# Optimization experiments

Hardware: AMD Instinct MI355X
Metric: run time of the kernel (lower is better)

The kernel has to match this reference:

```python
import jax, jax.numpy as jnp
import numpy as np
import math

JOINT_NAMES = ['pelvis', 'hip_R', 'hip_L', 'knee_R', 'knee_L', 'ankle_R', 'ankle_L', 'trunk', 'shoulder_R', 'shoulder_L', 'elbow_R', 'elbow_L']
KINEMATIC_CHAINS = {'pelvis': ['hip_R', 'hip_L', 'trunk'], 'hip_R': ['pelvis', 'knee_R'], 'hip_L': ['pelvis', 'knee_L'], 'knee_R': ['hip_R', 'ankle_R'], 'knee_L': ['hip_L', 'ankle_L'], 'ankle_R': ['knee_R'], 'ankle_L': ['knee_L'], 'trunk': ['pelvis', 'shoulder_R', 'shoulder_L'], 'shoulder_R': ['trunk', 'elbow_R'], 'shoulder_L': ['trunk', 'elbow_L'], 'elbow_R': ['shoulder_R'], 'elbow_L': ['shoulder_L']}

D_MODEL = 128
N_HEADS = 4
HEAD_DIM = D_MODEL // N_HEADS
B = 16384
N = 12

def build_adjacency_matrix():
    n = len(JOINT_NAMES)
    adj = np.zeros((n, n), dtype=np.float32)
    idx = {name: i for i, name in enumerate(JOINT_NAMES)}
    for joint, neighbors in KINEMATIC_CHAINS.items():
        i = idx[joint]
        for nb in neighbors:
            j = idx[nb]
            adj[i, j] = 1.0
            adj[j, i] = 1.0
    adj = adj + np.eye(n, dtype=np.float32)
    return jnp.asarray(adj)

def setup_inputs() -> dict:
    key = jax.random.key(0)
    ks = jax.random.split(key, 12)
    s = 1.0 / math.sqrt(D_MODEL)  # torch Linear default init scale
    inp = {
        'x': jax.random.normal(ks[0], (B, N, D_MODEL), dtype=jnp.float32),
        'visibility': jax.random.uniform(ks[1], (B, N), dtype=jnp.float32),
        'Wq': jax.random.uniform(ks[2], (D_MODEL, D_MODEL), jnp.float32, -s, s),
        'bq': jax.random.uniform(ks[3], (D_MODEL,), jnp.float32, -s, s),
        'Wk': jax.random.uniform(ks[4], (D_MODEL, D_MODEL), jnp.float32, -s, s),
        'bk': jax.random.uniform(ks[5], (D_MODEL,), jnp.float32, -s, s),
        'Wv': jax.random.uniform(ks[6], (D_MODEL, D_MODEL), jnp.float32, -s, s),
        'bv': jax.random.uniform(ks[7], (D_MODEL,), jnp.float32, -s, s),
        'Wo': jax.random.uniform(ks[8], (D_MODEL, D_MODEL), jnp.float32, -s, s),
        'bo': jax.random.uniform(ks[9], (D_MODEL,), jnp.float32, -s, s),
        'bias_scale': jnp.asarray(1.0, dtype=jnp.float32),
        'adjacency': build_adjacency_matrix(),
    }
    return inp

def reference(x, visibility, Wq, bq, Wk, bk, Wv, bv, Wo, bo, bias_scale, adjacency):
    Bsz, Nj, D = x.shape
    # projections; weights stored as (out,in) like torch Linear -> x @ W.T + b
    def proj(W, b):
        return (jnp.einsum('bnd,ed->bne', x, W) + b).reshape(Bsz, Nj, N_HEADS, HEAD_DIM).transpose(0, 2, 1, 3)
    q = proj(Wq, bq)  # (B, H, N, hd)
    k = proj(Wk, bk)
    v = proj(Wv, bv)
    scores = jnp.einsum('bhnd,bhmd->bhnm', q, k) / math.sqrt(HEAD_DIM)
    scores = scores + adjacency[None, None, :, :] * bias_scale
    # visibility mask: subtract 10 where key joint is not visible
    scores = scores - 10.0 * (1.0 - visibility[:, None, None, :])
    attn = jax.nn.softmax(scores, axis=-1)
    out = jnp.einsum('bhnm,bhmd->bhnd', attn, v)
    out = out.transpose(0, 2, 1, 3).reshape(Bsz, Nj, D)
    out = jnp.einsum('bnd,ed->bne', out, Wo) + bo
    return out
```

## Files before the change

### kernel.cpp

```cpp
#include <hip/hip_runtime.h>


typedef unsigned short u16;
typedef short bf16x8 __attribute__((ext_vector_type(8)));
typedef short bf16x4 __attribute__((ext_vector_type(4)));
typedef float f32x4 __attribute__((ext_vector_type(4)));

#define MFMA(a, b, c) __builtin_amdgcn_mfma_f32_16x16x32_bf16((a), (b), (c), 0, 0, 0)

#define BPW   4
#define ROWS  (BPW * 12)
#define XPAD  136
#define VPAD  20
#define PPAD  20

struct SMem {
    u16   qs[ROWS * XPAD];
    u16   ks[ROWS * XPAD];
    u16   vT[BPW * 128 * VPAD];
    u16   P[4 * 16 * PPAD];
    float bias_s[16 * 16];
    float vis_s[BPW * 16];
    float bvec[4 * 128];
    float rls[4 * 16];
};

__device__ __forceinline__ u16 f2b(float f) {
    unsigned u = __builtin_bit_cast(unsigned, f);
    return (u16)((u + 0x7fffu + ((u >> 16) & 1u)) >> 16);
}

__device__ __forceinline__ void st4(u16* p, float a, float b, float c, float d) {
    ushort4 v; v.x = f2b(a); v.y = f2b(b); v.z = f2b(c); v.w = f2b(d);
    *(ushort4*)p = v;
}

__device__ __forceinline__ bf16x8 pack8(float4 a, float4 b) {
    bf16x8 r;
    r[0] = (short)f2b(a.x); r[1] = (short)f2b(a.y);
    r[2] = (short)f2b(a.z); r[3] = (short)f2b(a.w);
    r[4] = (short)f2b(b.x); r[5] = (short)f2b(b.y);
    r[6] = (short)f2b(b.z); r[7] = (short)f2b(b.w);
    return r;
}

__global__ void prep_w(const float* __restrict__ Wq, const float* __restrict__ Wk,
                       const float* __restrict__ Wv, const float* __restrict__ Wo,
                       u16* __restrict__ wbf) {
    int i = blockIdx.x * 256 + threadIdx.x;
    wbf[i]         = f2b(Wq[i]);
    wbf[16384 + i] = f2b(Wk[i]);
    wbf[32768 + i] = f2b(Wv[i]);
    wbf[49152 + i] = f2b(Wo[i]);
}

__global__ __launch_bounds__(256, 3) void cja_main(
    const float* __restrict__ x, const float* __restrict__ vis,
    const float* __restrict__ bq, const float* __restrict__ bk,
    const float* __restrict__ bv, const float* __restrict__ bo,
    const float* __restrict__ bias_scale, const float* __restrict__ adj,
    const u16* __restrict__ wbf, float* __restrict__ out)
{
    extern __shared__ char smraw[];
    SMem& sm = *(SMem*)smraw;

    const int tid  = threadIdx.x;
    const int wave = tid >> 6;
    const int lane = tid & 63;
    const int lq   = lane >> 4;
    const int lm   = lane & 15;
    const int b0   = blockIdx.x * BPW;

    for (int i = tid; i < BPW * 128; i += 256) {
        unsigned* d = (unsigned*)(sm.vT + i * VPAD + 12);
        d[0] = 0u; d[1] = 0u; d[2] = 0u; d[3] = 0u;
    }
    {
        const float L2E = 1.4426950408889634f;
        float scale = bias_scale[0] * L2E;
        int n = tid >> 4, m = tid & 15;
        float bval;
        if (m >= 12)     bval = -1e30f;
        else if (n < 12) bval = adj[n * 12 + m] * scale;
        else             bval = 0.0f;
        sm.bias_s[tid] = bval;
        if (tid < BPW * 16) {
            int bb = tid >> 4, mm = tid & 15;
            sm.vis_s[tid] = (mm < 12) ? 10.0f * L2E * (1.0f - vis[(size_t)(b0 + bb) * 12 + mm])
                                      : 0.0f;
        }
        if (tid < 128) {
            sm.bvec[tid]       = bq[tid];
            sm.bvec[128 + tid] = bk[tid];
            sm.bvec[256 + tid] = bv[tid];
            sm.bvec[384 + tid] = bo[tid];
        }
    }
    __syncthreads();

    {
        const u16* Wq_b = wbf;
        const u16* Wk_b = wbf + 16384;
        const u16* Wv_b = wbf + 32768;
        const float* xw = x + (size_t)b0 * 1536;
        f32x4 accq[2][3], acck[2][3], accv[3][2];
        #pragma unroll
        for (int i = 0; i < 2; i++)
            #pragma unroll
            for (int j = 0; j < 3; j++) { accq[i][j] = (f32x4){0,0,0,0}; acck[i][j] = (f32x4){0,0,0,0}; }
        #pragma unroll
        for (int i = 0; i < 3; i++)
            #pragma unroll
            for (int j = 0; j < 2; j++) accv[i][j] = (f32x4){0,0,0,0};

        const int mrow0 = wave * 32 + lm;
        const int mrow1 = mrow0 + 16;
        #pragma unroll
        for (int ks2 = 0; ks2 < 4; ks2++) {
            const int koff = ks2 * 32 + lq * 8;
            bf16x8 xf[3];
            #pragma unroll
            for (int nt = 0; nt < 3; nt++) {
                const float* xp = xw + (nt * 16 + lm) * 128 + koff;
                float4 u0 = *(const float4*)xp;
                float4 u1 = *(const float4*)(xp + 4);
                xf[nt] = pack8(u0, u1);
            }
            bf16x8 wq0 = *(const bf16x8*)(Wq_b + mrow0 * 128 + koff);
            bf16x8 wq1 = *(const bf16x8*)(Wq_b + mrow1 * 128 + koff);
            bf16x8 wk0 = *(const bf16x8*)(Wk_b + mrow0 * 128 + koff);
            bf16x8 wk1 = *(const bf16x8*)(Wk_b + mrow1 * 128 + koff);
            bf16x8 wv0 = *(const bf16x8*)(Wv_b + mrow0 * 128 + koff);
            bf16x8 wv1 = *(const bf16x8*)(Wv_b + mrow1 * 128 + koff);
            #pragma unroll
            for (int nt = 0; nt < 3; nt++) {
                accq[0][nt] = MFMA(wq0, xf[nt], accq[0][nt]);
                accq[1][nt] = MFMA(wq1, xf[nt], accq[1][nt]);
                acck[0][nt] = MFMA(wk0, xf[nt], acck[0][nt]);
                acck[1][nt] = MFMA(wk1, xf[nt], acck[1][nt]);
                accv[nt][0] = MFMA(xf[nt], wv0, accv[nt][0]);
                accv[nt][1] = MFMA(xf[nt], wv1, accv[nt][1]);
            }
        }
        #pragma unroll
        for (int mi = 0; mi < 2; mi++) {
            const int e0 = (wave * 2 + mi) * 16 + lq * 4;
            float bq0 = sm.bvec[e0], bq1 = sm.bvec[e0+1], bq2 = sm.bvec[e0+2], bq3 = sm.bvec[e0+3];
            float bk0 = sm.bvec[128+e0], bk1 = sm.bvec[128+e0+1], bk2 = sm.bvec[128+e0+2], bk3 = sm.bvec[128+e0+3];
            #pragma unroll
            for (int nt = 0; nt < 3; nt++) {
                const int n = nt * 16 + lm;
                st4(sm.qs + n * XPAD + e0, accq[mi][nt][0]+bq0, accq[mi][nt][1]+bq1,
                                           accq[mi][nt][2]+bq2, accq[mi][nt][3]+bq3);
                st4(sm.ks + n * XPAD + e0, acck[mi][nt][0]+bk0, acck[mi][nt][1]+bk1,
                                           acck[mi][nt][2]+bk2, acck[mi][nt][3]+bk3);
            }
        }
        #pragma unroll
        for (int nt2 = 0; nt2 < 2; nt2++) {
            const int e = (wave * 2 + nt2) * 16 + lm;
            const float bvv = sm.bvec[256 + e];
            #pragma unroll
            for (int mt = 0; mt < 3; mt++) {
                #pragma unroll
                for (int r = 0; r < 4; r++) {
                    int n = mt * 16 + lq * 4 + r;
                    int bb = n / 12, j = n - bb * 12;
                    sm.vT[bb * (128 * VPAD) + e * VPAD + j] = f2b(accv[mt][nt2][r] + bvv);
                }
            }
        }
    }
    __syncthreads();

    {
        const int bl   = wave;
        const int nql  = (lm < 12) ? lm : 11;
        const u16* qrowp = sm.qs + (bl * 12 + nql) * XPAD;
        const u16* krowp = sm.ks + (bl * 12 + nql) * XPAD;
        const float vism = sm.vis_s[bl * 16 + lm];
        float bias_b[4];
        #pragma unroll
        for (int r = 0; r < 4; r++) bias_b[r] = sm.bias_s[(lq * 4 + r) * 16 + lm];
        u16*   Pw  = sm.P + wave * (16 * PPAD);
        float* rlw = sm.rls + wave * 16;
        const u16* vTb = sm.vT + bl * (128 * VPAD);
        const float SC2 = 0.2550348606381560f;
        const bf16x8 z8 = {0,0,0,0,0,0,0,0};
        #pragma unroll
        for (int h = 0; h < 4; h++) {
            bf16x8 qa = *(const bf16x8*)(qrowp + h * 32 + lq * 8);
            bf16x8 kb = *(const bf16x8*)(krowp + h * 32 + lq * 8);
            f32x4 sc = MFMA(qa, kb, ((f32x4){0,0,0,0}));
            #pragma unroll
            for (int r = 0; r < 4; r++) {
                float s2 = sc[r] * SC2 + bias_b[r] - vism;
                float e  = __builtin_amdgcn_exp2f(s2);
                float l  = e;
                l += __shfl_xor(l, 1, 16);
                l += __shfl_xor(l, 2, 16);
                l += __shfl_xor(l, 4, 16);
                l += __shfl_xor(l, 8, 16);
                Pw[(lq * 4 + r) * PPAD + lm] = f2b(e);
                if (lm == 0) rlw[lq * 4 + r] = __builtin_amdgcn_rcpf(l);
            }
            float rln = rlw[lm];
            bf16x8 pb = z8;
            if (lq < 2) {
                const bf16x4* pp = (const bf16x4*)(Pw + lm * PPAD + lq * 8);
                pb = __builtin_shufflevector(pp[0], pp[1], 0, 1, 2, 3, 4, 5, 6, 7);
            }
            #pragma unroll
            for (int mt = 0; mt < 2; mt++) {
                bf16x8 va = z8;
                if (lq < 2) {
                    const bf16x4* vp = (const bf16x4*)(vTb + (h * 32 + mt * 16 + lm) * VPAD + lq * 8);
                    va = __builtin_shufflevector(vp[0], vp[1], 0, 1, 2, 3, 4, 5, 6, 7);
                }
                f32x4 c = MFMA(va, pb, ((f32x4){0,0,0,0}));
                if (lm < 12) {
                    u16* d = sm.qs + (bl * 12 + lm) * XPAD + h * 32 + mt * 16 + lq * 4;
                    st4(d, c[0] * rln, c[1] * rln, c[2] * rln, c[3] * rln);
                }
            }
        }
    }
    __syncthreads();

    {
        const u16* Wo_b = wbf + 49152;
        f32x4 acc[2][3];
        #pragma unroll
        for (int i = 0; i < 2; i++)
            #pragma unroll
            for (int j = 0; j < 3; j++) acc[i][j] = (f32x4){0,0,0,0};
        const int m0 = wave * 32 + lm;
        #pragma unroll
        for (int ks2 = 0; ks2 < 4; ks2++) {
            const int koff = ks2 * 32 + lq * 8;
            bf16x8 a0 = *(const bf16x8*)(Wo_b + m0 * 128 + koff);
            bf16x8 a1 = *(const bf16x8*)(Wo_b + (m0 + 16) * 128 + koff);
            #pragma unroll
            for (int nt = 0; nt < 3; nt++) {
                bf16x8 bfr = *(const bf16x8*)(sm.qs + (nt * 16 + lm) * XPAD + koff);
                acc[0][nt] = MFMA(a0, bfr, acc[0][nt]);
                acc[1][nt] = MFMA(a1, bfr, acc[1][nt]);
            }
        }
        #pragma unroll
        for (int mi = 0; mi < 2; mi++) {
            const int e0 = (wave * 2 + mi) * 16 + lq * 4;
            float bo0 = sm.bvec[384+e0], bo1 = sm.bvec[384+e0+1],
                  bo2 = sm.bvec[384+e0+2], bo3 = sm.bvec[384+e0+3];
            #pragma unroll
            for (int nt = 0; nt < 3; nt++) {
                const int n = nt * 16 + lm;
                float4 o;
                o.x = acc[mi][nt][0] + bo0;
                o.y = acc[mi][nt][1] + bo1;
                o.z = acc[mi][nt][2] + bo2;
                o.w = acc[mi][nt][3] + bo3;
                *(float4*)(out + ((size_t)(b0 * 12 + n) << 7) + e0) = o;
            }
        }
    }
}

extern "C" void kernel_launch(void* const* d_in, const int* in_sizes, int n_in,
                              void* d_out, int out_size, void* d_ws, size_t ws_size,
                              hipStream_t stream) {
    const float* x   = (const float*)d_in[0];
    const float* vis = (const float*)d_in[1];
    const float* Wq  = (const float*)d_in[2];
    const float* bq  = (const float*)d_in[3];
    const float* Wk  = (const float*)d_in[4];
    const float* bk  = (const float*)d_in[5];
    const float* Wv  = (const float*)d_in[6];
    const float* bv  = (const float*)d_in[7];
    const float* Wo  = (const float*)d_in[8];
    const float* bo  = (const float*)d_in[9];
    const float* bs  = (const float*)d_in[10];
    const float* adj = (const float*)d_in[11];
    u16* wbf = (u16*)d_ws;

    prep_w<<<64, 256, 0, stream>>>(Wq, Wk, Wv, Wo, wbf);
    cja_main<<<16384 / BPW, 256, sizeof(SMem), stream>>>(
        x, vis, bq, bk, bv, bo, bs, adj, wbf, (float*)d_out);
}
```

Baseline: 287.2 us.

## Shrink shared memory, drop setup barrier, batch attention heads with swizzle reductions

Removes the shared-memory staging of biases, visibility and adjacency; each thread now loads these directly into registers, so the initial __syncthreads is gone. V transpose padding and the P buffer shrink, and P now reuses the K region, which reduces LDS per block and raises the launch-bounds occupancy target from 3 to 4. Attention scores for all four heads are computed together, softmax row sums use ds_swizzle instead of shfl, and normalization is applied before the PV MFMA, removing the per-head LDS round trip for reciprocals. The cost is higher register pressure, more redundant global loads of small parameters, and the risk of losing occupancy if the register count grows.

```diff
diff --git a/kernel.cpp b/kernel.cpp
--- a/kernel.cpp
+++ b/kernel.cpp
@@ -2,28 +2,25 @@
 
 
 typedef unsigned short u16;
+typedef unsigned int   u32;
 typedef short bf16x8 __attribute__((ext_vector_type(8)));
-typedef short bf16x4 __attribute__((ext_vector_type(4)));
-typedef float f32x4 __attribute__((ext_vector_type(4)));
+typedef float f32x4  __attribute__((ext_vector_type(4)));
 
 #define MFMA(a, b, c) __builtin_amdgcn_mfma_f32_16x16x32_bf16((a), (b), (c), 0, 0, 0)
 
 #define BPW   4
 #define ROWS  (BPW * 12)
 #define XPAD  136
-#define VPAD  20
-#define PPAD  20
+#define VPAD  14
+#define PPAD  24
 
 struct SMem {
-    u16   qs[ROWS * XPAD];
-    u16   ks[ROWS * XPAD];
-    u16   vT[BPW * 128 * VPAD];
-    u16   P[4 * 16 * PPAD];
-    float bias_s[16 * 16];
-    float vis_s[BPW * 16];
-    float bvec[4 * 128];
-    float rls[4 * 16];
+    u16 qs[ROWS * XPAD];
+    u16 ks[ROWS * XPAD];
+    u16 vT[BPW * 128 * VPAD];
 };
+
+#define SWZ(x, patt) __int_as_float(__builtin_amdgcn_ds_swizzle(__float_as_int(x), (patt)))
 
 __device__ __forceinline__ u16 f2b(float f) {
     unsigned u = __builtin_bit_cast(unsigned, f);
@@ -54,15 +51,14 @@
     wbf[49152 + i] = f2b(Wo[i]);
 }
 
-__global__ __launch_bounds__(256, 3) void cja_main(
+__global__ __launch_bounds__(256, 4) void cja_main(
     const float* __restrict__ x, const float* __restrict__ vis,
     const float* __restrict__ bq, const float* __restrict__ bk,
     const float* __restrict__ bv, const float* __restrict__ bo,
     const float* __restrict__ bias_scale, const float* __restrict__ adj,
     const u16* __restrict__ wbf, float* __restrict__ out)
 {
-    extern __shared__ char smraw[];
-    SMem& sm = *(SMem*)smraw;
+    __shared__ SMem sm;
 
     const int tid  = threadIdx.x;
     const int wave = tid >> 6;
@@ -71,32 +67,24 @@
     const int lm   = lane & 15;
     const int b0   = blockIdx.x * BPW;
 
-    for (int i = tid; i < BPW * 128; i += 256) {
-        unsigned* d = (unsigned*)(sm.vT + i * VPAD + 12);
-        d[0] = 0u; d[1] = 0u; d[2] = 0u; d[3] = 0u;
-    }
-    {
-        const float L2E = 1.4426950408889634f;
-        float scale = bias_scale[0] * L2E;
-        int n = tid >> 4, m = tid & 15;
-        float bval;
-        if (m >= 12)     bval = -1e30f;
-        else if (n < 12) bval = adj[n * 12 + m] * scale;
-        else             bval = 0.0f;
-        sm.bias_s[tid] = bval;
-        if (tid < BPW * 16) {
-            int bb = tid >> 4, mm = tid & 15;
-            sm.vis_s[tid] = (mm < 12) ? 10.0f * L2E * (1.0f - vis[(size_t)(b0 + bb) * 12 + mm])
-                                      : 0.0f;
-        }
-        if (tid < 128) {
-            sm.bvec[tid]       = bq[tid];
-            sm.bvec[128 + tid] = bk[tid];
-            sm.bvec[256 + tid] = bv[tid];
-            sm.bvec[384 + tid] = bo[tid];
-        }
-    }
-    __syncthreads();
+    #pragma unroll
+    for (int z = 0; z < 2; z++) {
+        int i = tid + z * 256;
+        *(u32*)(sm.vT + i * VPAD + 12) = 0u;
+    }
+
+    const float L2E = 1.4426950408889634f;
+    const float scale = bias_scale[0] * L2E;
+    float vv = 1.0f;
+    if (lm < 12) vv = vis[(size_t)(b0 + wave) * 12 + lm];
+    const float vism = 10.0f * L2E * (1.0f - vv);
+    float bias_b[4];
+    #pragma unroll
+    for (int r = 0; r < 4; r++) {
+        int n  = lq * 4 + r;
+        int nc = (n < 12) ? n : 11;
+        bias_b[r] = (lm < 12) ? adj[nc * 12 + lm] * scale : -1e30f;
+    }
 
     {
         const u16* Wq_b = wbf;
@@ -145,21 +133,21 @@
         #pragma unroll
         for (int mi = 0; mi < 2; mi++) {
             const int e0 = (wave * 2 + mi) * 16 + lq * 4;
-            float bq0 = sm.bvec[e0], bq1 = sm.bvec[e0+1], bq2 = sm.bvec[e0+2], bq3 = sm.bvec[e0+3];
-            float bk0 = sm.bvec[128+e0], bk1 = sm.bvec[128+e0+1], bk2 = sm.bvec[128+e0+2], bk3 = sm.bvec[128+e0+3];
+            float4 bq4 = *(const float4*)(bq + e0);
+            float4 bk4 = *(const float4*)(bk + e0);
             #pragma unroll
             for (int nt = 0; nt < 3; nt++) {
                 const int n = nt * 16 + lm;
-                st4(sm.qs + n * XPAD + e0, accq[mi][nt][0]+bq0, accq[mi][nt][1]+bq1,
-                                           accq[mi][nt][2]+bq2, accq[mi][nt][3]+bq3);
-                st4(sm.ks + n * XPAD + e0, acck[mi][nt][0]+bk0, acck[mi][nt][1]+bk1,
-                                           acck[mi][nt][2]+bk2, acck[mi][nt][3]+bk3);
+                st4(sm.qs + n * XPAD + e0, accq[mi][nt][0]+bq4.x, accq[mi][nt][1]+bq4.y,
+                                           accq[mi][nt][2]+bq4.z, accq[mi][nt][3]+bq4.w);
+                st4(sm.ks + n * XPAD + e0, acck[mi][nt][0]+bk4.x, acck[mi][nt][1]+bk4.y,
+                                           acck[mi][nt][2]+bk4.z, acck[mi][nt][3]+bk4.w);
             }
         }
         #pragma unroll
         for (int nt2 = 0; nt2 < 2; nt2++) {
             const int e = (wave * 2 + nt2) * 16 + lm;
-            const float bvv = sm.bvec[256 + e];
+            const float bvv = bv[e];
             #pragma unroll
             for (int mt = 0; mt < 3; mt++) {
                 #pragma unroll
@@ -178,49 +166,65 @@
         const int nql  = (lm < 12) ? lm : 11;
         const u16* qrowp = sm.qs + (bl * 12 + nql) * XPAD;
         const u16* krowp = sm.ks + (bl * 12 + nql) * XPAD;
-        const float vism = sm.vis_s[bl * 16 + lm];
-        float bias_b[4];
-        #pragma unroll
-        for (int r = 0; r < 4; r++) bias_b[r] = sm.bias_s[(lq * 4 + r) * 16 + lm];
-        u16*   Pw  = sm.P + wave * (16 * PPAD);
-        float* rlw = sm.rls + wave * 16;
+        u16* Pw = sm.ks + bl * 12 * XPAD;
         const u16* vTb = sm.vT + bl * (128 * VPAD);
         const float SC2 = 0.2550348606381560f;
         const bf16x8 z8 = {0,0,0,0,0,0,0,0};
+
+        bf16x8 qa[4], kb[4];
         #pragma unroll
         for (int h = 0; h < 4; h++) {
-            bf16x8 qa = *(const bf16x8*)(qrowp + h * 32 + lq * 8);
-            bf16x8 kb = *(const bf16x8*)(krowp + h * 32 + lq * 8);
-            f32x4 sc = MFMA(qa, kb, ((f32x4){0,0,0,0}));
+            qa[h] = *(const bf16x8*)(qrowp + h * 32 + lq * 8);
+            kb[h] = *(const bf16x8*)(krowp + h * 32 + lq * 8);
+        }
+        f32x4 sc[4];
+        #pragma unroll
+        for (int h = 0; h < 4; h++) sc[h] = MFMA(qa[h], kb[h], ((f32x4){0,0,0,0}));
+
+        float p[4][4];
+        #pragma unroll
+        for (int h = 0; h < 4; h++)
+            #pragma unroll
+            for (int r = 0; r < 4; r++)
+                p[h][r] = __builtin_amdgcn_exp2f(sc[h][r] * SC2 + bias_b[r] - vism);
+        #pragma unroll
+        for (int h = 0; h < 4; h++)
             #pragma unroll
             for (int r = 0; r < 4; r++) {
-                float s2 = sc[r] * SC2 + bias_b[r] - vism;
-                float e  = __builtin_amdgcn_exp2f(s2);
-                float l  = e;
-                l += __shfl_xor(l, 1, 16);
-                l += __shfl_xor(l, 2, 16);
-                l += __shfl_xor(l, 4, 16);
-                l += __shfl_xor(l, 8, 16);
-                Pw[(lq * 4 + r) * PPAD + lm] = f2b(e);
-                if (lm == 0) rlw[lq * 4 + r] = __builtin_amdgcn_rcpf(l);
-            }
-            float rln = rlw[lm];
+                float l = p[h][r];
+                l += SWZ(l, 0x041F);
+                l += SWZ(l, 0x081F);
+                l += SWZ(l, 0x101F);
+                l += SWZ(l, 0x201F);
+                p[h][r] *= __builtin_amdgcn_rcpf(l);
+            }
+        #pragma unroll
+        for (int h = 0; h < 4; h++)
+            #pragma unroll
+            for (int r = 0; r < 4; r++)
+                Pw[h * (16 * PPAD) + (lq * 4 + r) * PPAD + lm] = f2b(p[h][r]);
+
+        #pragma unroll
+        for (int h = 0; h < 4; h++) {
             bf16x8 pb = z8;
-            if (lq < 2) {
-                const bf16x4* pp = (const bf16x4*)(Pw + lm * PPAD + lq * 8);
-                pb = __builtin_shufflevector(pp[0], pp[1], 0, 1, 2, 3, 4, 5, 6, 7);
-            }
+            if (lq < 2)
+                pb = *(const bf16x8*)(Pw + h * (16 * PPAD) + lm * PPAD + lq * 8);
             #pragma unroll
             for (int mt = 0; mt < 2; mt++) {
                 bf16x8 va = z8;
                 if (lq < 2) {
-                    const bf16x4* vp = (const bf16x4*)(vTb + (h * 32 + mt * 16 + lm) * VPAD + lq * 8);
-                    va = __builtin_shufflevector(vp[0], vp[1], 0, 1, 2, 3, 4, 5, 6, 7);
+                    const u16* vp = vTb + (h * 32 + mt * 16 + lm) * VPAD + lq * 8;
+                    uint4 w;
+                    w.x = *(const u32*)(vp);
+                    w.y = *(const u32*)(vp + 2);
+                    w.z = *(const u32*)(vp + 4);
+                    w.w = *(const u32*)(vp + 6);
+                    va = __builtin_bit_cast(bf16x8, w);
                 }
                 f32x4 c = MFMA(va, pb, ((f32x4){0,0,0,0}));
                 if (lm < 12) {
                     u16* d = sm.qs + (bl * 12 + lm) * XPAD + h * 32 + mt * 16 + lq * 4;
-                    st4(d, c[0] * rln, c[1] * rln, c[2] * rln, c[3] * rln);
+                    st4(d, c[0], c[1], c[2], c[3]);
                 }
             }
         }
@@ -250,16 +254,15 @@
         #pragma unroll
         for (int mi = 0; mi < 2; mi++) {
             const int e0 = (wave * 2 + mi) * 16 + lq * 4;
-            float bo0 = sm.bvec[384+e0], bo1 = sm.bvec[384+e0+1],
-                  bo2 = sm.bvec[384+e0+2], bo3 = sm.bvec[384+e0+3];
+            float4 bo4 = *(const float4*)(bo + e0);
             #pragma unroll
             for (int nt = 0; nt < 3; nt++) {
                 const int n = nt * 16 + lm;
                 float4 o;
-                o.x = acc[mi][nt][0] + bo0;
-                o.y = acc[mi][nt][1] + bo1;
-                o.z = acc[mi][nt][2] + bo2;
-                o.w = acc[mi][nt][3] + bo3;
+                o.x = acc[mi][nt][0] + bo4.x;
+                o.y = acc[mi][nt][1] + bo4.y;
+                o.z = acc[mi][nt][2] + bo4.z;
+                o.w = acc[mi][nt][3] + bo4.w;
                 *(float4*)(out + ((size_t)(b0 * 12 + n) << 7) + e0) = o;
             }
         }
@@ -284,6 +287,6 @@
     u16* wbf = (u16*)d_ws;
 
     prep_w<<<64, 256, 0, stream>>>(Wq, Wk, Wv, Wo, wbf);
-    cja_main<<<16384 / BPW, 256, sizeof(SMem), stream>>>(
+    cja_main<<<16384 / BPW, 256, 0, stream>>>(
         x, vis, bq, bk, bv, bo, bs, adj, wbf, (float*)d_out);
 }
```

New measurement: 353.8 us. 1.23x slower.
